# Kernel optimization log

Hardware: AMD Instinct MI355X
Metric: run time of the kernel (lower is better)

The kernel has to match this reference:

```python
import jax, jax.numpy as jnp
import numpy as np

N_POINTS = 64
N_COLS = 500000
N_ANGS = N_POINTS * (N_POINTS - 1) // 2  # 2016


def setup_inputs() -> dict:
    key = jax.random.key(0)
    k1, k2 = jax.random.split(key)
    X = jax.random.normal(k1, (N_POINTS, N_COLS), dtype=jnp.float32)
    angles = 0.1 * jax.random.normal(k2, (N_ANGS,), dtype=jnp.float32)
    mus = jnp.ones((N_POINTS,), dtype=jnp.float32)
    return {"X": X, "angles": angles, "mus": mus}


def reference(X, angles, mus):
    # X: [n, m]; apply n(n-1)/2 sequential Givens rotations over row pairs
    # in order (iTop, iBtm) for iTop < iBtm, then scale rows by mus.
    # Original torch math per pair: vt' = c*vt - s*vb ; vb' = s*vt + c*vb.
    n = X.shape[0]
    top_np, btm_np = np.triu_indices(n, k=1)  # row-major order matches the double loop
    top = jnp.asarray(top_np, dtype=jnp.int32)
    btm = jnp.asarray(btm_np, dtype=jnp.int32)

    def step(Y, inp):
        a, it, ib = inp
        c = jnp.cos(a)
        s = jnp.sin(a)
        vt = Y[it]  # [m]
        vb = Y[ib]  # [m]
        Y = Y.at[it].set(c * vt - s * vb)
        Y = Y.at[ib].set(s * vt + c * vb)
        return Y, None

    Y, _ = jax.lax.scan(step, X, (angles, top, btm))
    return Y * mus[:, None]
```

## Files before the change

kernel.cpp:

```cpp
#include <hip/hip_runtime.h>

#define NPTS   64
#define NCOLS  500000
#define NANG   2016
#define NFULL  7812
#define BLOCKS 768
#define WSTRIDE (BLOCKS * 4)

typedef __attribute__((ext_vector_type(8))) short bf16x8;
typedef __attribute__((ext_vector_type(4))) float f32x4;

static __device__ __forceinline__ short f2bf(float f) {
    union { float f; unsigned u; } uf; uf.f = f;
    unsigned u = uf.u;
    unsigned r = (u + 0x7fffu + ((u >> 16) & 1u)) >> 16;
    return (short)r;
}

static __host__ __device__ constexpr int rotS(int i) { return 63 * i - i * (i - 1) / 2; }

template<int I0, int I1>
__device__ __forceinline__ void chunk_lds(const float2* __restrict__ csn,
                                          float* __restrict__ P, int lane) {
    float q[64 - I0];
#pragma unroll
    for (int r = I0; r < 64; ++r) q[r - I0] = (r == lane) ? 1.0f : 0.0f;

    int k = 0;
#pragma unroll
    for (int i = I0; i < I1; ++i) {
#pragma unroll
        for (int ib = i + 1; ib < 64; ++ib, ++k) {
            float c = csn[k].x, s = csn[k].y;
            float t = q[i - I0], b = q[ib - I0];
            q[ib - I0] = s * t + c * b;
            q[i - I0]  = c * t - s * b;
        }
        P[i * 64 + lane] = q[i - I0];
    }
#pragma unroll
    for (int r = 0; r < I0; ++r) P[r * 64 + lane] = (r == lane) ? 1.0f : 0.0f;
#pragma unroll
    for (int r = I1; r < 64; ++r) P[r * 64 + lane] = q[r - I0];
}

__global__ __launch_bounds__(256) void fused_ortho(const float* __restrict__ X,
                                                   const float* __restrict__ angles,
                                                   const float* __restrict__ mus,
                                                   float* __restrict__ out) {
    __shared__ __align__(16) float sm[12288];
    const int tid  = threadIdx.x;
    const int lane = tid & 63;
    const int wave = __builtin_amdgcn_readfirstlane(tid >> 6);

    float2* csn = (float2*)sm;
    for (int t = tid; t < NANG; t += 256) {
        float s, c;
        sincosf(angles[t], &s, &c);
        csn[t] = make_float2(c, s);
    }
    __syncthreads();

    float* P0 = sm + 4096;
    float* P1 = sm + 8192;
    if (wave == 0)      chunk_lds<0, 19>(csn, P0, lane);
    else if (wave == 1) chunk_lds<19, 63>(csn + rotS(19), P1, lane);
    __syncthreads();

    {
        float acc[16] = {0.f};
#pragma unroll 4
        for (int k0 = 0; k0 < 64; k0 += 4) {
            float lo0 = P0[(k0 + 0) * 64 + lane];
            float lo1 = P0[(k0 + 1) * 64 + lane];
            float lo2 = P0[(k0 + 2) * 64 + lane];
            float lo3 = P0[(k0 + 3) * 64 + lane];
#pragma unroll
            for (int r = 0; r < 16; ++r) {
                const f32x4 h = *(const f32x4*)&P1[(wave * 16 + r) * 64 + k0];
                acc[r] = fmaf(h[0], lo0, acc[r]);
                acc[r] = fmaf(h[1], lo1, acc[r]);
                acc[r] = fmaf(h[2], lo2, acc[r]);
                acc[r] = fmaf(h[3], lo3, acc[r]);
            }
        }
#pragma unroll
        for (int r = 0; r < 16; ++r)
            sm[(wave * 16 + r) * 64 + lane] = acc[r] * mus[wave * 16 + r];
    }
    __syncthreads();

    const int laneN = lane & 15;
    const int quad  = lane >> 4;

    bf16x8 afrag[4][2];
#pragma unroll
    for (int t = 0; t < 4; ++t) {
#pragma unroll
        for (int q = 0; q < 2; ++q) {
            const float* src = sm + (t * 16 + laneN) * 64 + q * 32 + quad * 8;
            bf16x8 f;
#pragma unroll
            for (int j = 0; j < 8; ++j) f[j] = f2bf(src[j]);
            afrag[t][q] = f;
        }
    }

    const int gw = blockIdx.x * 4 + wave;

    for (int s = gw; s < NFULL; s += WSTRIDE) {
        const long col0 = (long)s * 64 + 4 * laneN;
        const float* xb = X + col0;

        bf16x8 bfrag[4][2];
#pragma unroll
        for (int q = 0; q < 2; ++q) {
#pragma unroll
            for (int j = 0; j < 8; ++j) {
                const int kk = q * 32 + quad * 8 + j;
                f32x4 v = *(const f32x4*)(xb + (long)kk * NCOLS);
#pragma unroll
                for (int u = 0; u < 4; ++u)
                    bfrag[u][q][j] = f2bf(v[u]);
            }
        }

#pragma unroll
        for (int t = 0; t < 4; ++t) {
            f32x4 acc[4];
#pragma unroll
            for (int u = 0; u < 4; ++u) {
                f32x4 a = {0.f, 0.f, 0.f, 0.f};
                a = __builtin_amdgcn_mfma_f32_16x16x32_bf16(afrag[t][0], bfrag[u][0], a, 0, 0, 0);
                a = __builtin_amdgcn_mfma_f32_16x16x32_bf16(afrag[t][1], bfrag[u][1], a, 0, 0, 0);
                acc[u] = a;
            }
#pragma unroll
            for (int rr = 0; rr < 4; ++rr) {
                const int row = t * 16 + quad * 4 + rr;
                f32x4 o = { acc[0][rr], acc[1][rr], acc[2][rr], acc[3][rr] };
                __builtin_nontemporal_store(o, (f32x4*)(out + (long)row * NCOLS + col0));
            }
        }
    }

    if (gw < 2) {
        const int col = NFULL * 64 + gw * 16 + laneN;
        const float* xb = X + col;
        bf16x8 bfrag[2];
#pragma unroll
        for (int q = 0; q < 2; ++q) {
            bf16x8 f;
#pragma unroll
            for (int j = 0; j < 8; ++j)
                f[j] = f2bf(xb[(long)(q * 32 + quad * 8 + j) * NCOLS]);
            bfrag[q] = f;
        }
#pragma unroll
        for (int t = 0; t < 4; ++t) {
            f32x4 a = {0.f, 0.f, 0.f, 0.f};
            a = __builtin_amdgcn_mfma_f32_16x16x32_bf16(afrag[t][0], bfrag[0], a, 0, 0, 0);
            a = __builtin_amdgcn_mfma_f32_16x16x32_bf16(afrag[t][1], bfrag[1], a, 0, 0, 0);
#pragma unroll
            for (int rr = 0; rr < 4; ++rr)
                __builtin_nontemporal_store(a[rr],
                    out + (long)(t * 16 + quad * 4 + rr) * NCOLS + col);
        }
    }
}

extern "C" void kernel_launch(void* const* d_in, const int* in_sizes, int n_in,
                              void* d_out, int out_size, void* d_ws, size_t ws_size,
                              hipStream_t stream) {
    const float* X      = (const float*)d_in[0];
    const float* angles = (const float*)d_in[1];
    const float* mus    = (const float*)d_in[2];
    fused_ortho<<<BLOCKS, 256, 0, stream>>>(X, angles, mus, (float*)d_out);
}
```

Before: 322.0 us.

## Use 512-thread blocks and a rolled LDS-based rotation chain to cut registers

Blocks grow from 256 to 512 threads, launch bounds become (512,4), and the grid drops to 512 blocks with 8 waves each, so each wave owns 8 rows of the 64x64 matrix product. The fully unrolled register-array Givens chain becomes a rolled loop that reads and writes the P matrices in LDS. This lowers register pressure and code size so more waves fit per CU for the memory-bound streaming GEMM. The cost is a slower serial prologue per block, because every rotation now goes through LDS.

Measured after the change: 269.4 us. 16.3% less time.

```diff
diff --git a/kernel.cpp b/kernel.cpp
--- a/kernel.cpp
+++ b/kernel.cpp
@@ -4,8 +4,9 @@
 #define NCOLS  500000
 #define NANG   2016
 #define NFULL  7812
-#define BLOCKS 768
-#define WSTRIDE (BLOCKS * 4)
+#define TPB    512
+#define BLOCKS 512
+#define WSTRIDE (BLOCKS * 8)
 
 typedef __attribute__((ext_vector_type(8))) short bf16x8;
 typedef __attribute__((ext_vector_type(4))) float f32x4;
@@ -19,42 +20,36 @@
 
 static __host__ __device__ constexpr int rotS(int i) { return 63 * i - i * (i - 1) / 2; }
 
-template<int I0, int I1>
-__device__ __forceinline__ void chunk_lds(const float2* __restrict__ csn,
-                                          float* __restrict__ P, int lane) {
-    float q[64 - I0];
-#pragma unroll
-    for (int r = I0; r < 64; ++r) q[r - I0] = (r == lane) ? 1.0f : 0.0f;
-
+__device__ __forceinline__ void chain_rolled(const float2* __restrict__ csn,
+                                             float* __restrict__ P,
+                                             int lane, int I0, int I1) {
+    for (int r = 0; r < 64; ++r) P[r * 64 + lane] = (r == lane) ? 1.0f : 0.0f;
     int k = 0;
-#pragma unroll
+#pragma unroll 1
     for (int i = I0; i < I1; ++i) {
-#pragma unroll
+        float t = P[i * 64 + lane];
+#pragma unroll 4
         for (int ib = i + 1; ib < 64; ++ib, ++k) {
-            float c = csn[k].x, s = csn[k].y;
-            float t = q[i - I0], b = q[ib - I0];
-            q[ib - I0] = s * t + c * b;
-            q[i - I0]  = c * t - s * b;
+            float2 cs = csn[k];
+            float b = P[ib * 64 + lane];
+            P[ib * 64 + lane] = cs.y * t + cs.x * b;
+            t = cs.x * t - cs.y * b;
         }
-        P[i * 64 + lane] = q[i - I0];
+        P[i * 64 + lane] = t;
     }
-#pragma unroll
-    for (int r = 0; r < I0; ++r) P[r * 64 + lane] = (r == lane) ? 1.0f : 0.0f;
-#pragma unroll
-    for (int r = I1; r < 64; ++r) P[r * 64 + lane] = q[r - I0];
 }
 
-__global__ __launch_bounds__(256) void fused_ortho(const float* __restrict__ X,
-                                                   const float* __restrict__ angles,
-                                                   const float* __restrict__ mus,
-                                                   float* __restrict__ out) {
+__global__ __launch_bounds__(TPB, 4) void fused_ortho(const float* __restrict__ X,
+                                                      const float* __restrict__ angles,
+                                                      const float* __restrict__ mus,
+                                                      float* __restrict__ out) {
     __shared__ __align__(16) float sm[12288];
     const int tid  = threadIdx.x;
     const int lane = tid & 63;
     const int wave = __builtin_amdgcn_readfirstlane(tid >> 6);
 
     float2* csn = (float2*)sm;
-    for (int t = tid; t < NANG; t += 256) {
+    for (int t = tid; t < NANG; t += TPB) {
         float s, c;
         sincosf(angles[t], &s, &c);
         csn[t] = make_float2(c, s);
@@ -63,12 +58,13 @@
 
     float* P0 = sm + 4096;
     float* P1 = sm + 8192;
-    if (wave == 0)      chunk_lds<0, 19>(csn, P0, lane);
-    else if (wave == 1) chunk_lds<19, 63>(csn + rotS(19), P1, lane);
+    if (wave == 0)      chain_rolled(csn, P0, lane, 0, 19);
+    else if (wave == 1) chain_rolled(csn + rotS(19), P1, lane, 19, 63);
     __syncthreads();
 
     {
-        float acc[16] = {0.f};
+        const int row0 = wave * 8;
+        float acc[8] = {0.f};
 #pragma unroll 4
         for (int k0 = 0; k0 < 64; k0 += 4) {
             float lo0 = P0[(k0 + 0) * 64 + lane];
@@ -76,8 +72,8 @@
             float lo2 = P0[(k0 + 2) * 64 + lane];
             float lo3 = P0[(k0 + 3) * 64 + lane];
 #pragma unroll
-            for (int r = 0; r < 16; ++r) {
-                const f32x4 h = *(const f32x4*)&P1[(wave * 16 + r) * 64 + k0];
+            for (int r = 0; r < 8; ++r) {
+                const f32x4 h = *(const f32x4*)&P1[(row0 + r) * 64 + k0];
                 acc[r] = fmaf(h[0], lo0, acc[r]);
                 acc[r] = fmaf(h[1], lo1, acc[r]);
                 acc[r] = fmaf(h[2], lo2, acc[r]);
@@ -85,8 +81,8 @@
             }
         }
 #pragma unroll
-        for (int r = 0; r < 16; ++r)
-            sm[(wave * 16 + r) * 64 + lane] = acc[r] * mus[wave * 16 + r];
+        for (int r = 0; r < 8; ++r)
+            sm[(row0 + r) * 64 + lane] = acc[r] * mus[row0 + r];
     }
     __syncthreads();
 
@@ -106,7 +102,7 @@
         }
     }
 
-    const int gw = blockIdx.x * 4 + wave;
+    const int gw = blockIdx.x * 8 + wave;
 
     for (int s = gw; s < NFULL; s += WSTRIDE) {
         const long col0 = (long)s * 64 + 4 * laneN;
@@ -175,5 +171,5 @@
     const float* X      = (const float*)d_in[0];
     const float* angles = (const float*)d_in[1];
     const float* mus    = (const float*)d_in[2];
-    fused_ortho<<<BLOCKS, 256, 0, stream>>>(X, angles, mus, (float*)d_out);
+    fused_ortho<<<BLOCKS, TPB, 0, stream>>>(X, angles, mus, (float*)d_out);
 }
```
